# Kernel tuning notes

Hardware: AMD Instinct MI355X
Metric: run time of the kernel (lower is better)

## Reference

```python
import jax, jax.numpy as jnp
import numpy as np

SVL = 0.5        # spatial_volume_length
FVL = 0.86603    # frustum_volume_length
IMG = 256        # input_image_size
FD = 48          # frustum_volume_depth
FS = IMG // 8    # frustum_volume_size = 32


def grid_sample_3d(vol, grid):
    """Trilinear grid_sample, padding_mode='zeros', align_corners=True.
    vol: (B,C,Dv,Hv,Wv); grid: (B,D,H,W,3), last dim = (x,y,z) in [-1,1]
    where x indexes Wv, y indexes Hv, z indexes Dv. Returns (B,C,D,H,W)."""
    B, C, Dv, Hv, Wv = vol.shape
    sp = grid.shape[1:4]
    x = (grid[..., 0] + 1.0) * 0.5 * (Wv - 1)
    y = (grid[..., 1] + 1.0) * 0.5 * (Hv - 1)
    z = (grid[..., 2] + 1.0) * 0.5 * (Dv - 1)
    x0f, y0f, z0f = jnp.floor(x), jnp.floor(y), jnp.floor(z)
    xd, yd, zd = x - x0f, y - y0f, z - z0f
    x0, y0, z0 = x0f.astype(jnp.int32), y0f.astype(jnp.int32), z0f.astype(jnp.int32)
    vol_flat = vol.reshape(B, C, Dv * Hv * Wv)
    gather = jax.vmap(lambda vf, ix: vf[:, ix])  # (C,M),(K,) -> (C,K)
    out = jnp.zeros((B, C) + sp, vol.dtype)
    for dz in (0, 1):
        for dy in (0, 1):
            for dx in (0, 1):
                xi, yi, zi = x0 + dx, y0 + dy, z0 + dz
                valid = (xi >= 0) & (xi < Wv) & (yi >= 0) & (yi < Hv) & (zi >= 0) & (zi < Dv)
                w = ((xd if dx else 1.0 - xd)
                     * (yd if dy else 1.0 - yd)
                     * (zd if dz else 1.0 - zd))
                w = jnp.where(valid, w, 0.0)
                idx = ((jnp.clip(zi, 0, Dv - 1) * Hv + jnp.clip(yi, 0, Hv - 1)) * Wv
                       + jnp.clip(xi, 0, Wv - 1))
                g = gather(vol_flat, idx.reshape(B, -1)).reshape((B, C) + sp)
                out = out + w[:, None] * g
    return out


def setup_inputs() -> dict:
    key = jax.random.key(0)
    k1, k2, k3, k4 = jax.random.split(key, 4)
    B, N, TN, C, V = 2, 16, 8, 64, 32
    return {
        "spatial_volume": jax.random.normal(k1, (B, C, V, V, V), dtype=jnp.float32),
        "target_RT": jax.random.normal(k2, (B, N, 3, 4), dtype=jnp.float32),
        "target_K": jax.random.normal(k3, (B, N, 4, 4), dtype=jnp.float32),
        "target_indices": jax.random.randint(k4, (B, TN), 0, N),
    }


def reference(spatial_volume, target_RT, target_K, target_indices):
    B, C, V = spatial_volume.shape[0], spatial_volume.shape[1], spatial_volume.shape[2]
    TN = target_indices.shape[1]
    BT = B * TN
    H = W = FS
    D = FD
    dt = spatial_volume.dtype

    # camera centers: -R^T t, distances to origin
    R = target_RT[..., :3, :3]                  # B,N,3,3
    T = target_RT[..., :3, 3]                   # B,N,3
    cam_pos = -jnp.einsum('bnji,bnj->bni', R, T)
    cam_dist = jnp.linalg.norm(cam_pos, axis=-1)  # B,N

    # gather per-target-view pose / K / distance
    bidx = jnp.arange(B)[:, None]
    poses = target_RT[bidx, target_indices].reshape(BT, 3, 4)
    Ks = target_K[bidx, target_indices].reshape(BT, 4, 4)
    dist = cam_dist[bidx, target_indices].reshape(BT)
    near, far = dist - FVL, dist + FVL

    # per-ray depth values (constant across pixels since near/far are scalar per view)
    tlin = jnp.linspace(0.0, 1.0, D, dtype=dt)
    depth = near[:, None] + tlin[None, :] * (far - near)[:, None]   # BT,D

    # pixel grid at frustum resolution, scaled to input-image pixel coords
    ys, xs = jnp.meshgrid(jnp.arange(H, dtype=dt), jnp.arange(W, dtype=dt), indexing='ij')
    pix = jnp.stack([xs, ys, jnp.ones_like(xs)], 0).reshape(1, 3, H * W)
    scale = jnp.array([IMG / FS, IMG / FS, 1.0], dtype=dt).reshape(1, 3, 1)
    pix = pix * scale                                                # 1,3,HW
    pts = pix[:, :, None, :] * depth[:, None, :, None]               # BT,3,D,HW

    # unproject homogeneous image points through inverse(K @ [R|t])
    P = jnp.einsum('bij,bjk->bik', Ks[:, :3, :3], poses)             # BT,3,4
    bottom = jnp.broadcast_to(jnp.array([0.0, 0.0, 0.0, 1.0], dtype=dt).reshape(1, 1, 4), (BT, 1, 4))
    P4 = jnp.concatenate([P, bottom], axis=1)
    Pinv = jnp.linalg.inv(P4)
    xyz = jnp.einsum('bij,bjk->bik', Pinv[:, :3, :3], pts.reshape(BT, 3, D * H * W)) + Pinv[:, :3, 3:]

    # normalize world coords to [-1,1] of the spatial volume and sample
    grid = (xyz / SVL).reshape(BT, 3, D, H, W).transpose(0, 2, 3, 4, 1)  # BT,D,H,W,3
    sv = jnp.broadcast_to(spatial_volume[:, None], (B, TN, C, V, V, V)).reshape(BT, C, V, V, V)
    feats = grid_sample_3d(sv, grid)                                  # BT,C,D,H,W
    depth_vol = jnp.broadcast_to(depth[:, :, None, None], (BT, D, H, W))
    return feats, depth_vol
```

## Files before the change

### kernel.cpp

```cpp
#include <hip/hip_runtime.h>
#include <cstdint>

#define BB   2
#define NN   16
#define TNN  8
#define BT   16
#define CC   64
#define VV   32
#define V3   (VV*VV*VV)
#define DD   48
#define HH   32
#define WW   32
#define FVL_ 0.86603

__global__ void setup_params(const float* __restrict__ RT, const float* __restrict__ Km,
                             const int* __restrict__ tidx, float* __restrict__ params) {
    int bt = threadIdx.x;
    if (bt >= BT) return;
    int b = bt / TNN, j = bt % TNN;
    int n = tidx[b * TNN + j];
    const float* pose = RT + (size_t)(b * NN + n) * 12;
    const float* K    = Km + (size_t)(b * NN + n) * 16;

    double T0 = pose[3], T1 = pose[7], T2 = pose[11];
    double cp0 = -((double)pose[0] * T0 + (double)pose[4] * T1 + (double)pose[8]  * T2);
    double cp1 = -((double)pose[1] * T0 + (double)pose[5] * T1 + (double)pose[9]  * T2);
    double cp2 = -((double)pose[2] * T0 + (double)pose[6] * T1 + (double)pose[10] * T2);
    double dist = sqrt(cp0*cp0 + cp1*cp1 + cp2*cp2);
    double nearv = dist - FVL_;
    double step  = 2.0 * FVL_ / (DD - 1);

    double A[3][3], bv[3];
    #pragma unroll
    for (int i = 0; i < 3; ++i) {
        #pragma unroll
        for (int jj = 0; jj < 3; ++jj)
            A[i][jj] = (double)K[i*4+0]*pose[0*4+jj] + (double)K[i*4+1]*pose[1*4+jj]
                     + (double)K[i*4+2]*pose[2*4+jj];
        bv[i] = (double)K[i*4+0]*pose[3] + (double)K[i*4+1]*pose[7] + (double)K[i*4+2]*pose[11];
    }
    double c00 =  A[1][1]*A[2][2] - A[1][2]*A[2][1];
    double c01 =  A[1][2]*A[2][0] - A[1][0]*A[2][2];
    double c02 =  A[1][0]*A[2][1] - A[1][1]*A[2][0];
    double det = A[0][0]*c00 + A[0][1]*c01 + A[0][2]*c02;
    double Mi[3][3];
    Mi[0][0] = c00 / det;
    Mi[0][1] = (A[0][2]*A[2][1] - A[0][1]*A[2][2]) / det;
    Mi[0][2] = (A[0][1]*A[1][2] - A[0][2]*A[1][1]) / det;
    Mi[1][0] = c01 / det;
    Mi[1][1] = (A[0][0]*A[2][2] - A[0][2]*A[2][0]) / det;
    Mi[1][2] = (A[0][2]*A[1][0] - A[0][0]*A[1][2]) / det;
    Mi[2][0] = c02 / det;
    Mi[2][1] = (A[0][1]*A[2][0] - A[0][0]*A[2][1]) / det;
    Mi[2][2] = (A[0][0]*A[1][1] - A[0][1]*A[1][0]) / det;
    double tv[3];
    #pragma unroll
    for (int i = 0; i < 3; ++i)
        tv[i] = -(Mi[i][0]*bv[0] + Mi[i][1]*bv[1] + Mi[i][2]*bv[2]);

    const double s = 31.0;
    float* p = params + bt * 16;
    #pragma unroll
    for (int i = 0; i < 3; ++i) {
        p[i*4+0] = (float)(s * Mi[i][0] * 8.0);
        p[i*4+1] = (float)(s * Mi[i][1] * 8.0);
        p[i*4+2] = (float)(s * Mi[i][2]);
        p[i*4+3] = (float)(s * tv[i] + 15.5);
    }
    p[12] = (float)nearv;
    p[13] = (float)step;
}

__global__ __launch_bounds__(256) void transpose_vol(const float* __restrict__ vol,
                                                     float* __restrict__ volT) {
    int idx = blockIdx.x * 256 + threadIdx.x;
    int c    = idx & 63;
    int rest = idx >> 6;
    int zyx  = rest & (V3 - 1);
    int b    = rest >> 15;
    volT[(((size_t)b * V3 + zyx) << 6) | c] = vol[((size_t)(b * CC + c) * V3) + zyx];
}

template<bool CHLAST>
__global__ __launch_bounds__(512) void sample_kernel(const float* __restrict__ vol,
                                                     const float* __restrict__ params,
                                                     float* __restrict__ feats,
                                                     float* __restrict__ depthv) {
    int w  = threadIdx.x;
    int ty = threadIdx.y;
    int blk = blockIdx.x;
    int h  = blk & 31;
    int t2 = blk >> 5;
    int d  = t2 % DD;
    int bt = t2 / DD;
    int b  = bt >> 3;

    const float* p = params + bt * 16;
    float depth = fmaf(p[13], (float)d, p[12]);
    float fw = (float)w, fh = (float)h;
    float cx = fmaf(depth, fmaf(p[0], fw, fmaf(p[1], fh, p[2])),  p[3]);
    float cy = fmaf(depth, fmaf(p[4], fw, fmaf(p[5], fh, p[6])),  p[7]);
    float cz = fmaf(depth, fmaf(p[8], fw, fmaf(p[9], fh, p[10])), p[11]);

    float acc0 = 0.f, acc1 = 0.f, acc2 = 0.f, acc3 = 0.f;
    bool inside = (cx > -1.f) && (cx < 32.f) && (cy > -1.f) && (cy < 32.f)
               && (cz > -1.f) && (cz < 32.f);
    if (inside) {
        float xf = floorf(cx), yf = floorf(cy), zf = floorf(cz);
        int x0 = (int)xf, y0 = (int)yf, z0 = (int)zf;
        float xd = cx - xf, yd = cy - yf, zd = cz - zf;
        int x0c = max(x0, 0), x1c = min(x0 + 1, 31);
        int y0c = max(y0, 0), y1c = min(y0 + 1, 31);
        int z0c = max(z0, 0), z1c = min(z0 + 1, 31);
        float wx0 = (x0     >= 0) ? 1.f - xd : 0.f;
        float wx1 = (x0 + 1 <= 31) ? xd      : 0.f;
        float wy0 = (y0     >= 0) ? 1.f - yd : 0.f;
        float wy1 = (y0 + 1 <= 31) ? yd      : 0.f;
        float wz0 = (z0     >= 0) ? 1.f - zd : 0.f;
        float wz1 = (z0 + 1 <= 31) ? zd      : 0.f;

        if constexpr (CHLAST) {
            const size_t base = (size_t)b * ((size_t)V3 * 64) + (size_t)(ty << 2);
            #define CORNER(zc, yc, xc, WGT) do {                                         \
                const float4 v = *reinterpret_cast<const float4*>(                        \
                    vol + base + (((((size_t)(zc)) * 32 + (yc)) * 32 + (xc)) << 6));      \
                float wg = (WGT);                                                         \
                acc0 = fmaf(wg, v.x, acc0);  acc1 = fmaf(wg, v.y, acc1);                  \
                acc2 = fmaf(wg, v.z, acc2);  acc3 = fmaf(wg, v.w, acc3);                  \
            } while (0)
            CORNER(z0c, y0c, x0c, wz0 * wy0 * wx0);
            CORNER(z0c, y0c, x1c, wz0 * wy0 * wx1);
            CORNER(z0c, y1c, x0c, wz0 * wy1 * wx0);
            CORNER(z0c, y1c, x1c, wz0 * wy1 * wx1);
            CORNER(z1c, y0c, x0c, wz1 * wy0 * wx0);
            CORNER(z1c, y0c, x1c, wz1 * wy0 * wx1);
            CORNER(z1c, y1c, x0c, wz1 * wy1 * wx0);
            CORNER(z1c, y1c, x1c, wz1 * wy1 * wx1);
            #undef CORNER
        } else {
            int o000 = ((z0c * 32) + y0c) * 32 + x0c;
            int o001 = ((z0c * 32) + y0c) * 32 + x1c;
            int o010 = ((z0c * 32) + y1c) * 32 + x0c;
            int o011 = ((z0c * 32) + y1c) * 32 + x1c;
            int o100 = ((z1c * 32) + y0c) * 32 + x0c;
            int o101 = ((z1c * 32) + y0c) * 32 + x1c;
            int o110 = ((z1c * 32) + y1c) * 32 + x0c;
            int o111 = ((z1c * 32) + y1c) * 32 + x1c;
            float w000 = wz0*wy0*wx0, w001 = wz0*wy0*wx1, w010 = wz0*wy1*wx0, w011 = wz0*wy1*wx1;
            float w100 = wz1*wy0*wx0, w101 = wz1*wy0*wx1, w110 = wz1*wy1*wx0, w111 = wz1*wy1*wx1;
            float accs[4] = {0.f, 0.f, 0.f, 0.f};
            #pragma unroll
            for (int k = 0; k < 4; ++k) {
                const float* vc = vol + (size_t)(b * CC + (ty << 2) + k) * V3;
                float a = 0.f;
                a = fmaf(w000, vc[o000], a); a = fmaf(w001, vc[o001], a);
                a = fmaf(w010, vc[o010], a); a = fmaf(w011, vc[o011], a);
                a = fmaf(w100, vc[o100], a); a = fmaf(w101, vc[o101], a);
                a = fmaf(w110, vc[o110], a); a = fmaf(w111, vc[o111], a);
                accs[k] = a;
            }
            acc0 = accs[0]; acc1 = accs[1]; acc2 = accs[2]; acc3 = accs[3];
        }
    }

    const size_t CH = (size_t)DD * HH * WW;
    size_t o = (((size_t)bt * CC + (ty << 2)) * DD + d) * (HH * WW) + h * WW + w;
    feats[o]          = acc0;
    feats[o + CH]     = acc1;
    feats[o + 2 * CH] = acc2;
    feats[o + 3 * CH] = acc3;
    if (ty == 0)
        depthv[((size_t)bt * DD + d) * (HH * WW) + h * WW + w] = depth;
}

extern "C" void kernel_launch(void* const* d_in, const int* in_sizes, int n_in,
                              void* d_out, int out_size, void* d_ws, size_t ws_size,
                              hipStream_t stream) {
    const float* vol  = (const float*)d_in[0];
    const float* RT   = (const float*)d_in[1];
    const float* Km   = (const float*)d_in[2];
    const int*   tidx = (const int*)d_in[3];

    float* feats  = (float*)d_out;
    float* depthv = feats + (size_t)BT * CC * DD * HH * WW;

    float* params = (float*)d_ws;
    float* volT   = (float*)((char*)d_ws + 4096);
    const size_t volT_bytes = (size_t)BB * CC * V3 * sizeof(float);
    bool use_cl = ws_size >= 4096 + volT_bytes;

    setup_params<<<1, 64, 0, stream>>>(RT, Km, tidx, params);
    if (use_cl) {
        transpose_vol<<<(BB * CC * V3) / 256, 256, 0, stream>>>(vol, volT);
        sample_kernel<true><<<BT * DD * HH, dim3(32, 16, 1), 0, stream>>>(volT, params, feats, depthv);
    } else {
        sample_kernel<false><<<BT * DD * HH, dim3(32, 16, 1), 0, stream>>>(vol, params, feats, depthv);
    }
}
```

Measured before the change: 237.8 us.

## Tile volume transpose through LDS and coalesce channel-last gathers per voxel

The channel-last transpose now stages 64x64 tiles in shared memory, so both its global reads and writes are coalesced instead of one side being strided. The sampling kernel remaps threads so 16 consecutive lanes read one voxel's 64 channels as contiguous float4 loads. Results are then re-transposed through LDS so feature stores stay coalesced along w. The cost is an extra barrier and shared-memory traffic per block.

```diff
diff --git a/kernel.cpp b/kernel.cpp
--- a/kernel.cpp
+++ b/kernel.cpp
@@ -71,23 +71,33 @@
     p[13] = (float)step;
 }
 
-__global__ __launch_bounds__(256) void transpose_vol(const float* __restrict__ vol,
-                                                     float* __restrict__ volT) {
-    int idx = blockIdx.x * 256 + threadIdx.x;
-    int c    = idx & 63;
-    int rest = idx >> 6;
-    int zyx  = rest & (V3 - 1);
-    int b    = rest >> 15;
-    volT[(((size_t)b * V3 + zyx) << 6) | c] = vol[((size_t)(b * CC + c) * V3) + zyx];
-}
-
-template<bool CHLAST>
-__global__ __launch_bounds__(512) void sample_kernel(const float* __restrict__ vol,
-                                                     const float* __restrict__ params,
-                                                     float* __restrict__ feats,
-                                                     float* __restrict__ depthv) {
-    int w  = threadIdx.x;
-    int ty = threadIdx.y;
+__global__ __launch_bounds__(256) void transpose_vol2(const float* __restrict__ vol,
+                                                      float* __restrict__ volT) {
+    __shared__ float tl[64 * 65];
+    int b    = blockIdx.x >> 9;
+    int tile = blockIdx.x & 511;
+    size_t zyx0 = (size_t)tile << 6;
+    int l  = threadIdx.x & 63;
+    int gq = threadIdx.x >> 6;
+    #pragma unroll
+    for (int k = 0; k < 16; ++k) {
+        int c = (gq << 4) + k;
+        tl[l * 65 + c] = vol[(((size_t)(b * 64 + c)) << 15) + zyx0 + l];
+    }
+    __syncthreads();
+    #pragma unroll
+    for (int k = 0; k < 16; ++k) {
+        int zy = (gq << 4) + k;
+        volT[((size_t)b << 21) + ((zyx0 + zy) << 6) + l] = tl[zy * 65 + l];
+    }
+}
+
+__global__ __launch_bounds__(512) void sample_cl2(const float* __restrict__ volT,
+                                                  const float* __restrict__ params,
+                                                  float* __restrict__ feats,
+                                                  float* __restrict__ depthv) {
+    __shared__ float lds[32 * 68];
+    int t   = threadIdx.x;
     int blk = blockIdx.x;
     int h  = blk & 31;
     int t2 = blk >> 5;
@@ -97,6 +107,13 @@
 
     const float* p = params + bt * 16;
     float depth = fmaf(p[13], (float)d, p[12]);
+
+    int lane = t & 63;
+    int wv   = t >> 6;
+    int pp   = lane >> 4;
+    int q    = lane & 15;
+    int w    = (wv << 2) | pp;
+
     float fw = (float)w, fh = (float)h;
     float cx = fmaf(depth, fmaf(p[0], fw, fmaf(p[1], fh, p[2])),  p[3]);
     float cy = fmaf(depth, fmaf(p[4], fw, fmaf(p[5], fh, p[6])),  p[7]);
@@ -112,63 +129,112 @@
         int x0c = max(x0, 0), x1c = min(x0 + 1, 31);
         int y0c = max(y0, 0), y1c = min(y0 + 1, 31);
         int z0c = max(z0, 0), z1c = min(z0 + 1, 31);
-        float wx0 = (x0     >= 0) ? 1.f - xd : 0.f;
-        float wx1 = (x0 + 1 <= 31) ? xd      : 0.f;
-        float wy0 = (y0     >= 0) ? 1.f - yd : 0.f;
-        float wy1 = (y0 + 1 <= 31) ? yd      : 0.f;
-        float wz0 = (z0     >= 0) ? 1.f - zd : 0.f;
-        float wz1 = (z0 + 1 <= 31) ? zd      : 0.f;
-
-        if constexpr (CHLAST) {
-            const size_t base = (size_t)b * ((size_t)V3 * 64) + (size_t)(ty << 2);
-            #define CORNER(zc, yc, xc, WGT) do {                                         \
-                const float4 v = *reinterpret_cast<const float4*>(                        \
-                    vol + base + (((((size_t)(zc)) * 32 + (yc)) * 32 + (xc)) << 6));      \
-                float wg = (WGT);                                                         \
-                acc0 = fmaf(wg, v.x, acc0);  acc1 = fmaf(wg, v.y, acc1);                  \
-                acc2 = fmaf(wg, v.z, acc2);  acc3 = fmaf(wg, v.w, acc3);                  \
-            } while (0)
-            CORNER(z0c, y0c, x0c, wz0 * wy0 * wx0);
-            CORNER(z0c, y0c, x1c, wz0 * wy0 * wx1);
-            CORNER(z0c, y1c, x0c, wz0 * wy1 * wx0);
-            CORNER(z0c, y1c, x1c, wz0 * wy1 * wx1);
-            CORNER(z1c, y0c, x0c, wz1 * wy0 * wx0);
-            CORNER(z1c, y0c, x1c, wz1 * wy0 * wx1);
-            CORNER(z1c, y1c, x0c, wz1 * wy1 * wx0);
-            CORNER(z1c, y1c, x1c, wz1 * wy1 * wx1);
-            #undef CORNER
-        } else {
-            int o000 = ((z0c * 32) + y0c) * 32 + x0c;
-            int o001 = ((z0c * 32) + y0c) * 32 + x1c;
-            int o010 = ((z0c * 32) + y1c) * 32 + x0c;
-            int o011 = ((z0c * 32) + y1c) * 32 + x1c;
-            int o100 = ((z1c * 32) + y0c) * 32 + x0c;
-            int o101 = ((z1c * 32) + y0c) * 32 + x1c;
-            int o110 = ((z1c * 32) + y1c) * 32 + x0c;
-            int o111 = ((z1c * 32) + y1c) * 32 + x1c;
-            float w000 = wz0*wy0*wx0, w001 = wz0*wy0*wx1, w010 = wz0*wy1*wx0, w011 = wz0*wy1*wx1;
-            float w100 = wz1*wy0*wx0, w101 = wz1*wy0*wx1, w110 = wz1*wy1*wx0, w111 = wz1*wy1*wx1;
-            float accs[4] = {0.f, 0.f, 0.f, 0.f};
-            #pragma unroll
-            for (int k = 0; k < 4; ++k) {
-                const float* vc = vol + (size_t)(b * CC + (ty << 2) + k) * V3;
-                float a = 0.f;
-                a = fmaf(w000, vc[o000], a); a = fmaf(w001, vc[o001], a);
-                a = fmaf(w010, vc[o010], a); a = fmaf(w011, vc[o011], a);
-                a = fmaf(w100, vc[o100], a); a = fmaf(w101, vc[o101], a);
-                a = fmaf(w110, vc[o110], a); a = fmaf(w111, vc[o111], a);
-                accs[k] = a;
-            }
-            acc0 = accs[0]; acc1 = accs[1]; acc2 = accs[2]; acc3 = accs[3];
+        float wx0 = (x0     >= 0)  ? 1.f - xd : 0.f;
+        float wx1 = (x0 + 1 <= 31) ? xd       : 0.f;
+        float wy0 = (y0     >= 0)  ? 1.f - yd : 0.f;
+        float wy1 = (y0 + 1 <= 31) ? yd       : 0.f;
+        float wz0 = (z0     >= 0)  ? 1.f - zd : 0.f;
+        float wz1 = (z0 + 1 <= 31) ? zd       : 0.f;
+
+        const float* vb = volT + (((size_t)b << 21)) + (q << 2);
+        #define CORNER(zc, yc, xc, WGT) do {                                        \
+            const float4 v = *reinterpret_cast<const float4*>(                       \
+                vb + ((((size_t)(zc) * 32 + (yc)) * 32 + (xc)) << 6));               \
+            float wg = (WGT);                                                        \
+            acc0 = fmaf(wg, v.x, acc0);  acc1 = fmaf(wg, v.y, acc1);                 \
+            acc2 = fmaf(wg, v.z, acc2);  acc3 = fmaf(wg, v.w, acc3);                 \
+        } while (0)
+        CORNER(z0c, y0c, x0c, wz0 * wy0 * wx0);
+        CORNER(z0c, y0c, x1c, wz0 * wy0 * wx1);
+        CORNER(z0c, y1c, x0c, wz0 * wy1 * wx0);
+        CORNER(z0c, y1c, x1c, wz0 * wy1 * wx1);
+        CORNER(z1c, y0c, x0c, wz1 * wy0 * wx0);
+        CORNER(z1c, y0c, x1c, wz1 * wy0 * wx1);
+        CORNER(z1c, y1c, x0c, wz1 * wy1 * wx0);
+        CORNER(z1c, y1c, x1c, wz1 * wy1 * wx1);
+        #undef CORNER
+    }
+
+    float4 av = {acc0, acc1, acc2, acc3};
+    *reinterpret_cast<float4*>(&lds[w * 68 + (q << 2)]) = av;
+    __syncthreads();
+
+    int w2 = t & 31;
+    int g  = t >> 5;
+    float4 rv = *reinterpret_cast<const float4*>(&lds[w2 * 68 + (g << 2)]);
+    const size_t CHs = (size_t)DD * HH * WW;
+    size_t o = (((size_t)(bt * CC + (g << 2)) * DD + d) * (HH * WW)) + h * WW + w2;
+    feats[o]           = rv.x;
+    feats[o + CHs]     = rv.y;
+    feats[o + 2 * CHs] = rv.z;
+    feats[o + 3 * CHs] = rv.w;
+    if (t < 32)
+        depthv[((size_t)bt * DD + d) * (HH * WW) + h * WW + t] = depth;
+}
+
+__global__ __launch_bounds__(512) void sample_fallback(const float* __restrict__ vol,
+                                                       const float* __restrict__ params,
+                                                       float* __restrict__ feats,
+                                                       float* __restrict__ depthv) {
+    int w  = threadIdx.x;
+    int ty = threadIdx.y;
+    int blk = blockIdx.x;
+    int h  = blk & 31;
+    int t2 = blk >> 5;
+    int d  = t2 % DD;
+    int bt = t2 / DD;
+    int b  = bt >> 3;
+
+    const float* p = params + bt * 16;
+    float depth = fmaf(p[13], (float)d, p[12]);
+    float fw = (float)w, fh = (float)h;
+    float cx = fmaf(depth, fmaf(p[0], fw, fmaf(p[1], fh, p[2])),  p[3]);
+    float cy = fmaf(depth, fmaf(p[4], fw, fmaf(p[5], fh, p[6])),  p[7]);
+    float cz = fmaf(depth, fmaf(p[8], fw, fmaf(p[9], fh, p[10])), p[11]);
+
+    float accs[4] = {0.f, 0.f, 0.f, 0.f};
+    bool inside = (cx > -1.f) && (cx < 32.f) && (cy > -1.f) && (cy < 32.f)
+               && (cz > -1.f) && (cz < 32.f);
+    if (inside) {
+        float xf = floorf(cx), yf = floorf(cy), zf = floorf(cz);
+        int x0 = (int)xf, y0 = (int)yf, z0 = (int)zf;
+        float xd = cx - xf, yd = cy - yf, zd = cz - zf;
+        int x0c = max(x0, 0), x1c = min(x0 + 1, 31);
+        int y0c = max(y0, 0), y1c = min(y0 + 1, 31);
+        int z0c = max(z0, 0), z1c = min(z0 + 1, 31);
+        float wx0 = (x0     >= 0)  ? 1.f - xd : 0.f;
+        float wx1 = (x0 + 1 <= 31) ? xd       : 0.f;
+        float wy0 = (y0     >= 0)  ? 1.f - yd : 0.f;
+        float wy1 = (y0 + 1 <= 31) ? yd       : 0.f;
+        float wz0 = (z0     >= 0)  ? 1.f - zd : 0.f;
+        float wz1 = (z0 + 1 <= 31) ? zd       : 0.f;
+        int o000 = ((z0c * 32) + y0c) * 32 + x0c;
+        int o001 = ((z0c * 32) + y0c) * 32 + x1c;
+        int o010 = ((z0c * 32) + y1c) * 32 + x0c;
+        int o011 = ((z0c * 32) + y1c) * 32 + x1c;
+        int o100 = ((z1c * 32) + y0c) * 32 + x0c;
+        int o101 = ((z1c * 32) + y0c) * 32 + x1c;
+        int o110 = ((z1c * 32) + y1c) * 32 + x0c;
+        int o111 = ((z1c * 32) + y1c) * 32 + x1c;
+        float w000 = wz0*wy0*wx0, w001 = wz0*wy0*wx1, w010 = wz0*wy1*wx0, w011 = wz0*wy1*wx1;
+        float w100 = wz1*wy0*wx0, w101 = wz1*wy0*wx1, w110 = wz1*wy1*wx0, w111 = wz1*wy1*wx1;
+        #pragma unroll
+        for (int k = 0; k < 4; ++k) {
+            const float* vc = vol + (size_t)(b * CC + (ty << 2) + k) * V3;
+            float a = 0.f;
+            a = fmaf(w000, vc[o000], a); a = fmaf(w001, vc[o001], a);
+            a = fmaf(w010, vc[o010], a); a = fmaf(w011, vc[o011], a);
+            a = fmaf(w100, vc[o100], a); a = fmaf(w101, vc[o101], a);
+            a = fmaf(w110, vc[o110], a); a = fmaf(w111, vc[o111], a);
+            accs[k] = a;
         }
     }
-
-    const size_t CH = (size_t)DD * HH * WW;
+    const size_t CHs = (size_t)DD * HH * WW;
     size_t o = (((size_t)bt * CC + (ty << 2)) * DD + d) * (HH * WW) + h * WW + w;
-    feats[o]          = acc0;
-    feats[o + CH]     = acc1;
-    feats[o + 2 * CH] = acc2;
-    feats[o + 3 * CH] = acc3;
+    feats[o]           = accs[0];
+    feats[o + CHs]     = accs[1];
+    feats[o + 2 * CHs] = accs[2];
+    feats[o + 3 * CHs] = accs[3];
     if (ty == 0)
         depthv[((size_t)bt * DD + d) * (HH * WW) + h * WW + w] = depth;
 }
@@ -191,9 +257,9 @@
 
     setup_params<<<1, 64, 0, stream>>>(RT, Km, tidx, params);
     if (use_cl) {
-        transpose_vol<<<(BB * CC * V3) / 256, 256, 0, stream>>>(vol, volT);
-        sample_kernel<true><<<BT * DD * HH, dim3(32, 16, 1), 0, stream>>>(volT, params, feats, depthv);
+        transpose_vol2<<<BB * (V3 / 64), 256, 0, stream>>>(vol, volT);
+        sample_cl2<<<BT * DD * HH, 512, 0, stream>>>(volT, params, feats, depthv);
     } else {
-        sample_kernel<false><<<BT * DD * HH, dim3(32, 16, 1), 0, stream>>>(vol, params, feats, depthv);
-    }
-}
+        sample_fallback<<<BT * DD * HH, dim3(32, 16, 1), 0, stream>>>(vol, params, feats, depthv);
+    }
+}
```

After: 220.8 us. 7.1% less time.
